# Kernel tuning notes

Hardware: AMD Instinct MI355X
Metric: run time of the kernel (lower is better)

The kernel has to match this reference:

```python
import jax, jax.numpy as jnp
import numpy as np

D_MODEL, FFN, N_EXP = 1024, 4096, 8
BS, L = 4, 2048


def setup_inputs() -> dict:
    key = jax.random.key(0)
    ks = jax.random.split(key, 7)
    s = 0.02
    return {
        "x": jax.random.normal(ks[0], (BS, L, D_MODEL), dtype=jnp.float32),
        "gate_w": s * jax.random.normal(ks[1], (D_MODEL, N_EXP), dtype=jnp.float32),
        "gate_b": jnp.zeros((N_EXP,), dtype=jnp.float32),
        "W1": s * jax.random.normal(ks[2], (N_EXP, D_MODEL, FFN), dtype=jnp.float32),
        "b1": jnp.zeros((N_EXP, FFN), dtype=jnp.float32),
        "W2": s * jax.random.normal(ks[3], (N_EXP, FFN, D_MODEL), dtype=jnp.float32),
        "b2": jnp.zeros((N_EXP, D_MODEL), dtype=jnp.float32),
    }


def reference(x, gate_w, gate_b, W1, b1, W2, b2):
    # gate logits [bs, l, E]; NOTE: original applies Softmax(dim=1) -> over seq dim
    logits = jnp.einsum("bld,de->ble", x, gate_w) + gate_b
    probs = jax.nn.softmax(logits, axis=1)  # faithful to nn.Softmax(dim=1)
    idx = jnp.argmax(probs, axis=-1)  # top-1 expert per token, [bs, l]
    # topk_weights are computed in the original but never applied to output.
    out = jnp.zeros_like(x)
    for e in range(N_EXP):  # fixed small expert loop (structurally distinct weights)
        h = jax.nn.gelu(jnp.einsum("bld,df->blf", x, W1[e]) + b1[e], approximate=False)
        y = jnp.einsum("blf,fd->bld", h, W2[e]) + b2[e]
        out = out + jnp.where((idx == e)[..., None], y, jnp.float32(0.0))
    return out
```

## Files before the change

### kernel.cpp

```cpp
#include <hip/hip_runtime.h>
#include <hip/hip_bf16.h>

typedef unsigned short u16;
typedef unsigned int u32;

using bf16x8 = __attribute__((ext_vector_type(8))) short;
using f32x4  = __attribute__((ext_vector_type(4))) float;

static constexpr int TOK  = 8192;
static constexpr int SEQ  = 2048;
static constexpr int DM   = 1024;
static constexpr int FF   = 4096;
static constexpr int NE   = 8;
static constexpr int MAXT = 72;
static constexpr int NT1  = FF/128;
static constexpr int NT2  = DM/128;

static constexpr size_t O_LOGITS = 0;
static constexpr size_t O_M      = 262144;
static constexpr size_t O_Z      = O_M + 128;
static constexpr size_t O_CNT    = O_Z + 128;
static constexpr size_t O_CUR    = O_CNT + 64;
static constexpr size_t O_OFF    = O_CUR + 64;
static constexpr size_t O_DESC   = 263168;
static constexpr size_t O_PERM   = 266240;
static constexpr size_t O_IDX    = 299008;
static constexpr size_t O_XG     = 524288;
static constexpr size_t O_W1T    = O_XG  + (size_t)TOK*DM*2;
static constexpr size_t O_W2T    = O_W1T + (size_t)NE*DM*FF*2;
static constexpr size_t O_H      = O_W2T + (size_t)NE*DM*FF*2;

__device__ __forceinline__ u16 f2bf(float f){
  __hip_bfloat16 h = __float2bfloat16(f);
  return *reinterpret_cast<u16*>(&h);
}

__device__ __forceinline__ void gld_lds16(const void* g, void* l){
  __builtin_amdgcn_global_load_lds((const __attribute__((address_space(1))) void*)g,
                                   (__attribute__((address_space(3))) void*)l, 16, 0, 0);
}

__device__ __forceinline__ float gelu_f(float v){
  float u = v * fmaf(v*v, 0.044715f, 1.0f) * 0.7978845608f;
  float ex = __builtin_amdgcn_exp2f(u * -2.885390082f);
  return v * __builtin_amdgcn_rcpf(1.0f + ex);
}

__global__ void k_gate(const float* __restrict__ x, const float* __restrict__ gw,
                       const float* __restrict__ gb, float* __restrict__ logits){
  __shared__ float sgw[DM*NE];
  for (int i = threadIdx.x; i < DM*NE; i += 256) sgw[i] = gw[i];
  __syncthreads();
  int wave = threadIdx.x >> 6, lane = threadIdx.x & 63;
  int t = blockIdx.x * 4 + wave;
  const float* xr = x + (size_t)t * DM;
  float acc[NE];
#pragma unroll
  for (int e = 0; e < NE; ++e) acc[e] = 0.f;
#pragma unroll
  for (int k = 0; k < 16; ++k){
    int d = k*64 + lane;
    float xv = xr[d];
    const float* g = &sgw[d*NE];
#pragma unroll
    for (int e = 0; e < NE; ++e) acc[e] = fmaf(xv, g[e], acc[e]);
  }
#pragma unroll
  for (int off = 32; off; off >>= 1)
#pragma unroll
    for (int e = 0; e < NE; ++e) acc[e] += __shfl_xor(acc[e], off);
  if (lane == 0){
#pragma unroll
    for (int e = 0; e < NE; ++e) logits[(size_t)t*NE + e] = acc[e] + gb[e];
  }
}

__global__ void k_lse(const float* __restrict__ logits, float* __restrict__ mOut,
                      float* __restrict__ zOut){
  int be = blockIdx.x;
  int b = be >> 3, e = be & 7;
  const float* base = logits + ((size_t)b*SEQ)*NE + e;
  float m = -INFINITY;
  for (int l = threadIdx.x; l < SEQ; l += 256) m = fmaxf(m, base[(size_t)l*NE]);
  __shared__ float red[8];
#pragma unroll
  for (int off = 32; off; off >>= 1) m = fmaxf(m, __shfl_xor(m, off));
  if ((threadIdx.x & 63) == 0) red[threadIdx.x >> 6] = m;
  __syncthreads();
  m = fmaxf(fmaxf(red[0], red[1]), fmaxf(red[2], red[3]));
  float s = 0.f;
  for (int l = threadIdx.x; l < SEQ; l += 256) s += expf(base[(size_t)l*NE] - m);
#pragma unroll
  for (int off = 32; off; off >>= 1) s += __shfl_xor(s, off);
  if ((threadIdx.x & 63) == 0) red[4 + (threadIdx.x >> 6)] = s;
  __syncthreads();
  if (threadIdx.x == 0){ mOut[be] = m; zOut[be] = red[4]+red[5]+red[6]+red[7]; }
}

__global__ void k_route(const float* __restrict__ logits, const float* __restrict__ m,
                        const float* __restrict__ z, u32* __restrict__ cnt,
                        int* __restrict__ idx){
  int t = blockIdx.x*256 + threadIdx.x;
  int b = t >> 11;
  const float* lr = logits + (size_t)t*NE;
  float best = -INFINITY; int be = 0;
#pragma unroll
  for (int e = 0; e < NE; ++e){
    float p = expf(lr[e] - m[b*NE + e]) / z[b*NE + e];
    if (p > best){ best = p; be = e; }
  }
  idx[t] = be;
  atomicAdd(&cnt[be], 1u);
}

__global__ void k_plan(const u32* __restrict__ cnt, int* __restrict__ off,
                       int4* __restrict__ desc, u32* __restrict__ cur){
  if (threadIdx.x == 0){
    int offs[NE+1]; int o = 0;
    for (int e = 0; e < NE; ++e){ offs[e] = o; o += (int)cnt[e]; }
    offs[NE] = o;
    int nt = 0;
    for (int e = 0; e < NE; ++e){
      int c = (int)cnt[e];
      for (int s = 0; s < c; s += 128)
        desc[nt++] = make_int4(e, offs[e] + s, min(128, c - s), 0);
      off[e] = offs[e]; cur[e] = 0u;
    }
    off[NE] = offs[NE];
    for (int i = nt; i < MAXT; ++i) desc[i] = make_int4(-1, 0, 0, 0);
  }
}

__global__ void k_scatter(const int* __restrict__ idx, const int* __restrict__ off,
                          u32* __restrict__ cur, int* __restrict__ perm){
  int t = blockIdx.x*256 + threadIdx.x;
  int e = idx[t];
  int pos = off[e] + (int)atomicAdd(&cur[e], 1u);
  perm[pos] = t;
}

__global__ void k_gather(const float* __restrict__ x, const int* __restrict__ perm,
                         u16* __restrict__ Xg){
  int p = blockIdx.x;
  int t = perm[p];
  const float4* src = (const float4*)(x + (size_t)t*DM);
  float4 v = src[threadIdx.x];
  uint2 o;
  o.x = (u32)f2bf(v.x) | ((u32)f2bf(v.y) << 16);
  o.y = (u32)f2bf(v.z) | ((u32)f2bf(v.w) << 16);
  *(uint2*)(Xg + (size_t)p*DM + threadIdx.x*4) = o;
}

__global__ void k_trans(const float* __restrict__ in, u16* __restrict__ out,
                        int R, int C){
  __shared__ float tile[64][65];
  int e = blockIdx.z;
  int r0 = blockIdx.x*64, c0 = blockIdx.y*64;
  const float* src = in + ((size_t)e*R + r0)*C + c0;
  int lr = threadIdx.x >> 4, lc = (threadIdx.x & 15) * 4;
#pragma unroll
  for (int i = 0; i < 4; ++i){
    float4 v = *(const float4*)(src + (size_t)(lr + i*16)*C + lc);
    tile[lr + i*16][lc+0] = v.x; tile[lr + i*16][lc+1] = v.y;
    tile[lr + i*16][lc+2] = v.z; tile[lr + i*16][lc+3] = v.w;
  }
  __syncthreads();
  u16* dst = out + ((size_t)e*C + c0)*R + r0;
#pragma unroll
  for (int i = 0; i < 4; ++i){
    int oc = lr + i*16;
    u16 a0 = f2bf(tile[lc+0][oc]);
    u16 a1 = f2bf(tile[lc+1][oc]);
    u16 a2 = f2bf(tile[lc+2][oc]);
    u16 a3 = f2bf(tile[lc+3][oc]);
    uint2 o; o.x = (u32)a0 | ((u32)a1 << 16); o.y = (u32)a2 | ((u32)a3 << 16);
    *(uint2*)(dst + (size_t)oc*R + lc) = o;
  }
}

__global__ __launch_bounds__(256) void k_ffn1(const u16* __restrict__ Xg,
    const u16* __restrict__ W1T, const float* __restrict__ b1,
    u16* __restrict__ H, const int4* __restrict__ desc){
  int pid = blockIdx.x;
  int pid_sw = (pid & 7) * (MAXT*NT1/8) + (pid >> 3);
  int mt = pid_sw % MAXT;
  int n0 = (pid_sw / MAXT) * 128;
  int4 dd = desc[mt];
  int e = dd.x; if (e < 0) return;
  int m0 = dd.y, valid = dd.z;
  __shared__ __align__(16) u16 lA[2][128*32];
  __shared__ __align__(16) u16 lB[2][128*32];
  int tid = threadIdx.x, lane = tid & 63, wave = tid >> 6;
  int wr = wave >> 1, wc = wave & 1;
  const u16* Bsrc = W1T + ((size_t)e*FF + n0)*DM;
  f32x4 acc[4][4] = {};

  auto stage = [&](int buf, int kt){
    int k0 = kt * 32;
#pragma unroll
    for (int i = 0; i < 2; ++i){
      int qbase = wave*512 + i*2048;
      int qe = qbase + lane*8;
      int row = qe >> 5, col = qe & 31;
      int rowg = m0 + row; if (rowg > TOK-1) rowg = TOK-1;
      gld_lds16(Xg + (size_t)rowg*DM + k0 + col, &lA[buf][qbase]);
      gld_lds16(Bsrc + (size_t)row*DM + k0 + col, &lB[buf][qbase]);
    }
  };

  stage(0, 0);
  __syncthreads();
  const int KT = DM / 32;
  for (int kt = 0; kt < KT; ++kt){
    int cur = kt & 1;
    if (kt + 1 < KT) stage(cur ^ 1, kt + 1);
    const u16* pa = &lA[cur][(wr*64 + (lane & 15))*32 + (lane >> 4)*8];
    const u16* pb = &lB[cur][(wc*64 + (lane & 15))*32 + (lane >> 4)*8];
    bf16x8 a[4], b[4];
#pragma unroll
    for (int m = 0; m < 4; ++m) a[m] = *(const bf16x8*)(pa + m*16*32);
#pragma unroll
    for (int n = 0; n < 4; ++n) b[n] = *(const bf16x8*)(pb + n*16*32);
#pragma unroll
    for (int m = 0; m < 4; ++m)
#pragma unroll
      for (int n = 0; n < 4; ++n)
        acc[m][n] = __builtin_amdgcn_mfma_f32_16x16x32_bf16(a[m], b[n], acc[m][n], 0, 0, 0);
    __syncthreads();
  }

#pragma unroll
  for (int n = 0; n < 4; ++n){
    int col = n0 + wc*64 + n*16 + (lane & 15);
    float bias = b1[(size_t)e*FF + col];
#pragma unroll
    for (int m = 0; m < 4; ++m){
      int rbase = wr*64 + m*16 + ((lane >> 4) << 2);
#pragma unroll
      for (int j = 0; j < 4; ++j){
        int rit = rbase + j;
        if (rit < valid){
          float v = acc[m][n][j] + bias;
          H[(size_t)(m0 + rit)*FF + col] = f2bf(gelu_f(v));
        }
      }
    }
  }
}

__global__ __launch_bounds__(256) void k_ffn2(const u16* __restrict__ H,
    const u16* __restrict__ W2T, const float* __restrict__ b2,
    float* __restrict__ out, const int4* __restrict__ desc,
    const int* __restrict__ perm){
  int pid = blockIdx.x;
  int pid_sw = (pid & 7) * (MAXT*NT2/8) + (pid >> 3);
  int mt = pid_sw % MAXT;
  int n0 = (pid_sw / MAXT) * 128;
  int4 dd = desc[mt];
  int e = dd.x; if (e < 0) return;
  int m0 = dd.y, valid = dd.z;
  __shared__ __align__(16) u16 lA[2][128*32];
  __shared__ __align__(16) u16 lB[2][128*32];
  int tid = threadIdx.x, lane = tid & 63, wave = tid >> 6;
  int wr = wave >> 1, wc = wave & 1;
  const u16* Bsrc = W2T + ((size_t)e*DM + n0)*FF;
  f32x4 acc[4][4] = {};

  auto stage = [&](int buf, int kt){
    int k0 = kt * 32;
#pragma unroll
    for (int i = 0; i < 2; ++i){
      int qbase = wave*512 + i*2048;
      int qe = qbase + lane*8;
      int row = qe >> 5, col = qe & 31;
      int rowg = m0 + row; if (rowg > TOK-1) rowg = TOK-1;
      gld_lds16(H + (size_t)rowg*FF + k0 + col, &lA[buf][qbase]);
      gld_lds16(Bsrc + (size_t)row*FF + k0 + col, &lB[buf][qbase]);
    }
  };

  stage(0, 0);
  __syncthreads();
  const int KT = FF / 32;
  for (int kt = 0; kt < KT; ++kt){
    int cur = kt & 1;
    if (kt + 1 < KT) stage(cur ^ 1, kt + 1);
    const u16* pa = &lA[cur][(wr*64 + (lane & 15))*32 + (lane >> 4)*8];
    const u16* pb = &lB[cur][(wc*64 + (lane & 15))*32 + (lane >> 4)*8];
    bf16x8 a[4], b[4];
#pragma unroll
    for (int m = 0; m < 4; ++m) a[m] = *(const bf16x8*)(pa + m*16*32);
#pragma unroll
    for (int n = 0; n < 4; ++n) b[n] = *(const bf16x8*)(pb + n*16*32);
#pragma unroll
    for (int m = 0; m < 4; ++m)
#pragma unroll
      for (int n = 0; n < 4; ++n)
        acc[m][n] = __builtin_amdgcn_mfma_f32_16x16x32_bf16(a[m], b[n], acc[m][n], 0, 0, 0);
    __syncthreads();
  }

#pragma unroll
  for (int m = 0; m < 4; ++m){
#pragma unroll
    for (int j = 0; j < 4; ++j){
      int rit = wr*64 + m*16 + ((lane >> 4) << 2) + j;
      if (rit < valid){
        int tok = perm[m0 + rit];
#pragma unroll
        for (int n = 0; n < 4; ++n){
          int col = n0 + wc*64 + n*16 + (lane & 15);
          out[(size_t)tok*DM + col] = acc[m][n][j] + b2[(size_t)e*DM + col];
        }
      }
    }
  }
}

extern "C" void kernel_launch(void* const* d_in, const int* in_sizes, int n_in,
                              void* d_out, int out_size, void* d_ws, size_t ws_size,
                              hipStream_t stream){
  const float* x   = (const float*)d_in[0];
  const float* gw  = (const float*)d_in[1];
  const float* gb  = (const float*)d_in[2];
  const float* W1  = (const float*)d_in[3];
  const float* b1  = (const float*)d_in[4];
  const float* W2  = (const float*)d_in[5];
  const float* b2  = (const float*)d_in[6];
  float* out = (float*)d_out;
  char* ws = (char*)d_ws;

  float* logits = (float*)(ws + O_LOGITS);
  float* mArr   = (float*)(ws + O_M);
  float* zArr   = (float*)(ws + O_Z);
  u32*   cnt    = (u32*)  (ws + O_CNT);
  u32*   cur    = (u32*)  (ws + O_CUR);
  int*   off    = (int*)  (ws + O_OFF);
  int4*  desc   = (int4*) (ws + O_DESC);
  int*   perm   = (int*)  (ws + O_PERM);
  int*   idx    = (int*)  (ws + O_IDX);
  u16*   Xg     = (u16*)  (ws + O_XG);
  u16*   W1T    = (u16*)  (ws + O_W1T);
  u16*   W2T    = (u16*)  (ws + O_W2T);
  u16*   Hbuf   = (u16*)  (ws + O_H);

  hipMemsetAsync(ws + O_CNT, 0, 128, stream);

  k_gate   <<<TOK/4, 256, 0, stream>>>(x, gw, gb, logits);
  k_lse    <<<32,    256, 0, stream>>>(logits, mArr, zArr);
  k_route  <<<TOK/256, 256, 0, stream>>>(logits, mArr, zArr, cnt, idx);
  k_plan   <<<1,     64,  0, stream>>>(cnt, off, desc, cur);
  k_scatter<<<TOK/256, 256, 0, stream>>>(idx, off, cur, perm);
  k_gather <<<TOK,   256, 0, stream>>>(x, perm, Xg);
  k_trans  <<<dim3(DM/64, FF/64, NE), 256, 0, stream>>>(W1, W1T, DM, FF);
  k_trans  <<<dim3(FF/64, DM/64, NE), 256, 0, stream>>>(W2, W2T, FF, DM);
  k_ffn1   <<<MAXT*NT1, 256, 0, stream>>>(Xg, W1T, b1, Hbuf, desc);
  k_ffn2   <<<MAXT*NT2, 256, 0, stream>>>(Hbuf, W2T, b2, out, desc, perm);
}
```

Baseline: 474.6 us.

## Enlarge FFN1 tiles to 256x256 with swizzled LDS and split-K FFN2

FFN1 moves to 256x256 output tiles with a 64-wide K step and 512 threads. It adds an XOR-swizzled LDS layout, a phased MFMA schedule with raw barriers and setprio, and a second tile descriptor list built from 256-row chunks. FFN2 splits K in two and accumulates into the output with atomic adds, after a new kernel prefills the output with the per-expert bias. The aim is more data reuse per tile in the large GEMM and more workgroups for the small-N second GEMM. The cost is larger LDS use, heavier padding waste on partial 256-row tiles, and atomic traffic on the output.

```diff
diff --git a/kernel.cpp b/kernel.cpp
--- a/kernel.cpp
+++ b/kernel.cpp
@@ -13,8 +13,11 @@
 static constexpr int FF   = 4096;
 static constexpr int NE   = 8;
 static constexpr int MAXT = 72;
-static constexpr int NT1  = FF/128;
+static constexpr int MAXT2= 40;
 static constexpr int NT2  = DM/128;
+static constexpr int KS2  = 2;
+static constexpr int NWG1 = MAXT2 * (FF/256);
+static constexpr int NWG2 = MAXT * NT2 * KS2;
 
 static constexpr size_t O_LOGITS = 0;
 static constexpr size_t O_M      = 262144;
@@ -23,6 +26,7 @@
 static constexpr size_t O_CUR    = O_CNT + 64;
 static constexpr size_t O_OFF    = O_CUR + 64;
 static constexpr size_t O_DESC   = 263168;
+static constexpr size_t O_DESC2  = 264320;
 static constexpr size_t O_PERM   = 266240;
 static constexpr size_t O_IDX    = 299008;
 static constexpr size_t O_XG     = 524288;
@@ -39,6 +43,9 @@
   __builtin_amdgcn_global_load_lds((const __attribute__((address_space(1))) void*)g,
                                    (__attribute__((address_space(3))) void*)l, 16, 0, 0);
 }
+
+#define BAR()    asm volatile("s_barrier" ::: "memory")
+#define WAITV0() asm volatile("s_waitcnt vmcnt(0)" ::: "memory")
 
 __device__ __forceinline__ float gelu_f(float v){
   float u = v * fmaf(v*v, 0.044715f, 1.0f) * 0.7978845608f;
@@ -114,20 +121,24 @@
 }
 
 __global__ void k_plan(const u32* __restrict__ cnt, int* __restrict__ off,
-                       int4* __restrict__ desc, u32* __restrict__ cur){
+                       int4* __restrict__ desc, int4* __restrict__ desc2,
+                       u32* __restrict__ cur){
   if (threadIdx.x == 0){
     int offs[NE+1]; int o = 0;
     for (int e = 0; e < NE; ++e){ offs[e] = o; o += (int)cnt[e]; }
     offs[NE] = o;
-    int nt = 0;
+    int nt = 0, nt2 = 0;
     for (int e = 0; e < NE; ++e){
       int c = (int)cnt[e];
       for (int s = 0; s < c; s += 128)
         desc[nt++] = make_int4(e, offs[e] + s, min(128, c - s), 0);
+      for (int s = 0; s < c; s += 256)
+        desc2[nt2++] = make_int4(e, offs[e] + s, min(256, c - s), 0);
       off[e] = offs[e]; cur[e] = 0u;
     }
     off[NE] = offs[NE];
-    for (int i = nt; i < MAXT; ++i) desc[i] = make_int4(-1, 0, 0, 0);
+    for (int i = nt;  i < MAXT;  ++i) desc[i]  = make_int4(-1, 0, 0, 0);
+    for (int i = nt2; i < MAXT2; ++i) desc2[i] = make_int4(-1, 0, 0, 0);
   }
 }
 
@@ -178,69 +189,105 @@
   }
 }
 
-__global__ __launch_bounds__(256) void k_ffn1(const u16* __restrict__ Xg,
+__global__ __launch_bounds__(512, 2) void k_ffn1(const u16* __restrict__ Xg,
     const u16* __restrict__ W1T, const float* __restrict__ b1,
-    u16* __restrict__ H, const int4* __restrict__ desc){
+    u16* __restrict__ H, const int4* __restrict__ desc2){
   int pid = blockIdx.x;
-  int pid_sw = (pid & 7) * (MAXT*NT1/8) + (pid >> 3);
-  int mt = pid_sw % MAXT;
-  int n0 = (pid_sw / MAXT) * 128;
-  int4 dd = desc[mt];
+  int pid_sw = (pid & 7) * (NWG1/8) + (pid >> 3);
+  int mt = pid_sw % MAXT2;
+  int n0 = (pid_sw / MAXT2) * 256;
+  int4 dd = desc2[mt];
   int e = dd.x; if (e < 0) return;
   int m0 = dd.y, valid = dd.z;
-  __shared__ __align__(16) u16 lA[2][128*32];
-  __shared__ __align__(16) u16 lB[2][128*32];
+
+  __shared__ __align__(16) u16 lA[2][256*64];
+  __shared__ __align__(16) u16 lB[2][256*64];
+
   int tid = threadIdx.x, lane = tid & 63, wave = tid >> 6;
-  int wr = wave >> 1, wc = wave & 1;
+  int wm = wave >> 2, wn = wave & 3;
   const u16* Bsrc = W1T + ((size_t)e*FF + n0)*DM;
-  f32x4 acc[4][4] = {};
-
-  auto stage = [&](int buf, int kt){
-    int k0 = kt * 32;
-#pragma unroll
-    for (int i = 0; i < 2; ++i){
-      int qbase = wave*512 + i*2048;
-      int qe = qbase + lane*8;
-      int row = qe >> 5, col = qe & 31;
-      int rowg = m0 + row; if (rowg > TOK-1) rowg = TOK-1;
-      gld_lds16(Xg + (size_t)rowg*DM + k0 + col, &lA[buf][qbase]);
-      gld_lds16(Bsrc + (size_t)row*DM + k0 + col, &lB[buf][qbase]);
+
+  f32x4 acc[8][4] = {};
+  bf16x8 a[4][2], b0[2][2], b1r[2][2];
+
+  int srow = lane >> 3;
+  int cole = ((lane & 7) ^ srow) << 3;
+
+  auto STAGE = [&](int buf, int kt){
+    int k0 = kt * 64;
+    char* dA = (char*)&lA[buf][0];
+    char* dB = (char*)&lB[buf][0];
+#pragma unroll
+    for (int c = 0; c < 4; ++c){
+      int ci = wave*4 + c;
+      int row = ci*8 + srow;
+      int ra = m0 + row; if (ra > TOK-1) ra = TOK-1;
+      gld_lds16(Xg   + (size_t)ra *DM + k0 + cole, dA + ci*1024);
+      gld_lds16(Bsrc + (size_t)row*DM + k0 + cole, dB + ci*1024);
     }
   };
-
-  stage(0, 0);
-  __syncthreads();
-  const int KT = DM / 32;
+  auto LDA = [&](const u16* tb, int half){
+#pragma unroll
+    for (int f = 0; f < 4; ++f){
+      int R = wm*128 + half*64 + f*16 + (lane & 15);
+      int base = R*128 + (((lane >> 4)*16) ^ ((R & 7) << 4));
+      a[f][0] = *(const bf16x8*)((const char*)tb + base);
+      a[f][1] = *(const bf16x8*)((const char*)tb + (base ^ 64));
+    }
+  };
+  auto LDB = [&](const u16* tb, int half, bf16x8 (&b)[2][2]){
+#pragma unroll
+    for (int f = 0; f < 2; ++f){
+      int R = wn*64 + half*32 + f*16 + (lane & 15);
+      int base = R*128 + (((lane >> 4)*16) ^ ((R & 7) << 4));
+      b[f][0] = *(const bf16x8*)((const char*)tb + base);
+      b[f][1] = *(const bf16x8*)((const char*)tb + (base ^ 64));
+    }
+  };
+  auto MM = [&](int mh, int nh, bf16x8 (&b)[2][2]){
+    __builtin_amdgcn_s_setprio(1);
+#pragma unroll
+    for (int f = 0; f < 4; ++f)
+#pragma unroll
+      for (int g = 0; g < 2; ++g){
+        acc[mh*4+f][nh*2+g] =
+          __builtin_amdgcn_mfma_f32_16x16x32_bf16(a[f][0], b[g][0], acc[mh*4+f][nh*2+g], 0,0,0);
+        acc[mh*4+f][nh*2+g] =
+          __builtin_amdgcn_mfma_f32_16x16x32_bf16(a[f][1], b[g][1], acc[mh*4+f][nh*2+g], 0,0,0);
+      }
+    __builtin_amdgcn_s_setprio(0);
+  };
+
+  STAGE(0, 0);
+  WAITV0(); BAR();
+  const int KT = DM / 64;
   for (int kt = 0; kt < KT; ++kt){
-    int cur = kt & 1;
-    if (kt + 1 < KT) stage(cur ^ 1, kt + 1);
-    const u16* pa = &lA[cur][(wr*64 + (lane & 15))*32 + (lane >> 4)*8];
-    const u16* pb = &lB[cur][(wc*64 + (lane & 15))*32 + (lane >> 4)*8];
-    bf16x8 a[4], b[4];
-#pragma unroll
-    for (int m = 0; m < 4; ++m) a[m] = *(const bf16x8*)(pa + m*16*32);
-#pragma unroll
-    for (int n = 0; n < 4; ++n) b[n] = *(const bf16x8*)(pb + n*16*32);
-#pragma unroll
-    for (int m = 0; m < 4; ++m)
-#pragma unroll
-      for (int n = 0; n < 4; ++n)
-        acc[m][n] = __builtin_amdgcn_mfma_f32_16x16x32_bf16(a[m], b[n], acc[m][n], 0, 0, 0);
-    __syncthreads();
-  }
-
-#pragma unroll
-  for (int n = 0; n < 4; ++n){
-    int col = n0 + wc*64 + n*16 + (lane & 15);
+    const u16* cA = &lA[kt & 1][0];
+    const u16* cB = &lB[kt & 1][0];
+    if (kt + 1 < KT) STAGE((kt & 1) ^ 1, kt + 1);
+    LDA(cA, 0); LDB(cB, 0, b0);
+    BAR(); MM(0, 0, b0);  BAR();
+    LDB(cB, 1, b1r);
+    BAR(); MM(0, 1, b1r); BAR();
+    LDA(cA, 1);
+    BAR(); MM(1, 1, b1r); BAR();
+    MM(1, 0, b0);
+    if (kt + 1 < KT) WAITV0();
+    BAR();
+  }
+
+#pragma unroll
+  for (int fn = 0; fn < 4; ++fn){
+    int col = n0 + wn*64 + fn*16 + (lane & 15);
     float bias = b1[(size_t)e*FF + col];
 #pragma unroll
-    for (int m = 0; m < 4; ++m){
-      int rbase = wr*64 + m*16 + ((lane >> 4) << 2);
+    for (int fm = 0; fm < 8; ++fm){
+      int rbase = wm*128 + fm*16 + ((lane >> 4) << 2);
 #pragma unroll
       for (int j = 0; j < 4; ++j){
         int rit = rbase + j;
         if (rit < valid){
-          float v = acc[m][n][j] + bias;
+          float v = acc[fm][fn][j] + bias;
           H[(size_t)(m0 + rit)*FF + col] = f2bf(gelu_f(v));
         }
       }
@@ -248,14 +295,23 @@
   }
 }
 
+__global__ void k_bias(const int* __restrict__ idx, const float* __restrict__ b2,
+                       float* __restrict__ out){
+  int t = blockIdx.x;
+  int e = idx[t];
+  float4 v = *(const float4*)(b2 + (size_t)e*DM + threadIdx.x*4);
+  *(float4*)(out + (size_t)t*DM + threadIdx.x*4) = v;
+}
+
 __global__ __launch_bounds__(256) void k_ffn2(const u16* __restrict__ H,
-    const u16* __restrict__ W2T, const float* __restrict__ b2,
-    float* __restrict__ out, const int4* __restrict__ desc,
-    const int* __restrict__ perm){
+    const u16* __restrict__ W2T, float* __restrict__ out,
+    const int4* __restrict__ desc, const int* __restrict__ perm){
   int pid = blockIdx.x;
-  int pid_sw = (pid & 7) * (MAXT*NT2/8) + (pid >> 3);
+  int pid_sw = (pid & 7) * (NWG2/8) + (pid >> 3);
   int mt = pid_sw % MAXT;
-  int n0 = (pid_sw / MAXT) * 128;
+  int rest = pid_sw / MAXT;
+  int n0 = (rest & 7) * 128;
+  int ks = rest >> 3;
   int4 dd = desc[mt];
   int e = dd.x; if (e < 0) return;
   int m0 = dd.y, valid = dd.z;
@@ -279,12 +335,12 @@
     }
   };
 
-  stage(0, 0);
+  const int k_beg = ks * 64, k_end = k_beg + 64;
+  stage(0, k_beg);
   __syncthreads();
-  const int KT = FF / 32;
-  for (int kt = 0; kt < KT; ++kt){
+  for (int kt = k_beg; kt < k_end; ++kt){
     int cur = kt & 1;
-    if (kt + 1 < KT) stage(cur ^ 1, kt + 1);
+    if (kt + 1 < k_end) stage(cur ^ 1, kt + 1);
     const u16* pa = &lA[cur][(wr*64 + (lane & 15))*32 + (lane >> 4)*8];
     const u16* pb = &lB[cur][(wc*64 + (lane & 15))*32 + (lane >> 4)*8];
     bf16x8 a[4], b[4];
@@ -310,7 +366,7 @@
 #pragma unroll
         for (int n = 0; n < 4; ++n){
           int col = n0 + wc*64 + n*16 + (lane & 15);
-          out[(size_t)tok*DM + col] = acc[m][n][j] + b2[(size_t)e*DM + col];
+          unsafeAtomicAdd(&out[(size_t)tok*DM + col], acc[m][n][j]);
         }
       }
     }
@@ -337,6 +393,7 @@
   u32*   cur    = (u32*)  (ws + O_CUR);
   int*   off    = (int*)  (ws + O_OFF);
   int4*  desc   = (int4*) (ws + O_DESC);
+  int4*  desc2  = (int4*) (ws + O_DESC2);
   int*   perm   = (int*)  (ws + O_PERM);
   int*   idx    = (int*)  (ws + O_IDX);
   u16*   Xg     = (u16*)  (ws + O_XG);
@@ -349,11 +406,12 @@
   k_gate   <<<TOK/4, 256, 0, stream>>>(x, gw, gb, logits);
   k_lse    <<<32,    256, 0, stream>>>(logits, mArr, zArr);
   k_route  <<<TOK/256, 256, 0, stream>>>(logits, mArr, zArr, cnt, idx);
-  k_plan   <<<1,     64,  0, stream>>>(cnt, off, desc, cur);
+  k_plan   <<<1,     64,  0, stream>>>(cnt, off, desc, desc2, cur);
   k_scatter<<<TOK/256, 256, 0, stream>>>(idx, off, cur, perm);
   k_gather <<<TOK,   256, 0, stream>>>(x, perm, Xg);
   k_trans  <<<dim3(DM/64, FF/64, NE), 256, 0, stream>>>(W1, W1T, DM, FF);
   k_trans  <<<dim3(FF/64, DM/64, NE), 256, 0, stream>>>(W2, W2T, FF, DM);
-  k_ffn1   <<<MAXT*NT1, 256, 0, stream>>>(Xg, W1T, b1, Hbuf, desc);
-  k_ffn2   <<<MAXT*NT2, 256, 0, stream>>>(Hbuf, W2T, b2, out, desc, perm);
-}
+  k_ffn1   <<<NWG1,  512, 0, stream>>>(Xg, W1T, b1, Hbuf, desc2);
+  k_bias   <<<TOK,   256, 0, stream>>>(idx, b2, out);
+  k_ffn2   <<<NWG2,  256, 0, stream>>>(Hbuf, W2T, out, desc, perm);
+}
```

Result: slower. 548.7 us (+15.6%).

## Split-K the second expert GEMM with atomic accumulation and rework block ordering

Applied to the files above, without the earlier changes.

The second FFN GEMM is split four ways along K, so the grid is four times larger and each block runs a quarter of the K loop. Partial sums go to the output with float atomic adds. The output is pre-filled with the b2 bias in the gather kernel. The first GEMM's block-to-tile mapping is changed so groups of 8 N-tiles share an M-tile, which targets L2 reuse, and the gate kernel's weights are laid out transposed to allow float4 loads. The cost is atomic traffic and non-deterministic summation order in the output.

```diff
diff --git a/kernel.cpp b/kernel.cpp
--- a/kernel.cpp
+++ b/kernel.cpp
@@ -13,8 +13,9 @@
 static constexpr int FF   = 4096;
 static constexpr int NE   = 8;
 static constexpr int MAXT = 72;
-static constexpr int NT1  = FF/128;
-static constexpr int NT2  = DM/128;
+static constexpr int KS2  = 4;
+static constexpr int NWG1 = MAXT * (FF/128);
+static constexpr int NWG2 = MAXT * (DM/128) * KS2;
 
 static constexpr size_t O_LOGITS = 0;
 static constexpr size_t O_M      = 262144;
@@ -48,22 +49,27 @@
 
 __global__ void k_gate(const float* __restrict__ x, const float* __restrict__ gw,
                        const float* __restrict__ gb, float* __restrict__ logits){
-  __shared__ float sgw[DM*NE];
-  for (int i = threadIdx.x; i < DM*NE; i += 256) sgw[i] = gw[i];
+  __shared__ float sgw[NE*DM];
+  for (int i = threadIdx.x; i < DM*NE; i += 256){
+    int d = i >> 3, e = i & 7;
+    sgw[e*DM + d] = gw[i];
+  }
   __syncthreads();
   int wave = threadIdx.x >> 6, lane = threadIdx.x & 63;
   int t = blockIdx.x * 4 + wave;
-  const float* xr = x + (size_t)t * DM;
+  const float4* xr = (const float4*)(x + (size_t)t * DM);
   float acc[NE];
 #pragma unroll
   for (int e = 0; e < NE; ++e) acc[e] = 0.f;
 #pragma unroll
-  for (int k = 0; k < 16; ++k){
-    int d = k*64 + lane;
-    float xv = xr[d];
-    const float* g = &sgw[d*NE];
-#pragma unroll
-    for (int e = 0; e < NE; ++e) acc[e] = fmaf(xv, g[e], acc[e]);
+  for (int k = 0; k < 4; ++k){
+    int v4 = k*64 + lane;
+    float4 v = xr[v4];
+#pragma unroll
+    for (int e = 0; e < NE; ++e){
+      const float4 g = *(const float4*)&sgw[e*DM + v4*4];
+      acc[e] = fmaf(v.x, g.x, fmaf(v.y, g.y, fmaf(v.z, g.z, fmaf(v.w, g.w, acc[e]))));
+    }
   }
 #pragma unroll
   for (int off = 32; off; off >>= 1)
@@ -140,15 +146,19 @@
 }
 
 __global__ void k_gather(const float* __restrict__ x, const int* __restrict__ perm,
-                         u16* __restrict__ Xg){
+                         const int* __restrict__ idx, const float* __restrict__ b2,
+                         u16* __restrict__ Xg, float* __restrict__ out){
   int p = blockIdx.x;
   int t = perm[p];
+  int e = idx[t];
   const float4* src = (const float4*)(x + (size_t)t*DM);
   float4 v = src[threadIdx.x];
   uint2 o;
   o.x = (u32)f2bf(v.x) | ((u32)f2bf(v.y) << 16);
   o.y = (u32)f2bf(v.z) | ((u32)f2bf(v.w) << 16);
   *(uint2*)(Xg + (size_t)p*DM + threadIdx.x*4) = o;
+  float4 bv = ((const float4*)(b2 + (size_t)e*DM))[threadIdx.x];
+  ((float4*)(out + (size_t)t*DM))[threadIdx.x] = bv;
 }
 
 __global__ void k_trans(const float* __restrict__ in, u16* __restrict__ out,
@@ -178,13 +188,16 @@
   }
 }
 
+
 __global__ __launch_bounds__(256) void k_ffn1(const u16* __restrict__ Xg,
     const u16* __restrict__ W1T, const float* __restrict__ b1,
     u16* __restrict__ H, const int4* __restrict__ desc){
   int pid = blockIdx.x;
-  int pid_sw = (pid & 7) * (MAXT*NT1/8) + (pid >> 3);
-  int mt = pid_sw % MAXT;
-  int n0 = (pid_sw / MAXT) * 128;
+  int pid_sw = (pid & 7) * (NWG1/8) + (pid >> 3);
+  int ng  = pid_sw / (MAXT*8);
+  int rem = pid_sw - ng*(MAXT*8);
+  int mt  = rem >> 3;
+  int n0  = (ng*8 + (rem & 7)) * 128;
   int4 dd = desc[mt];
   int e = dd.x; if (e < 0) return;
   int m0 = dd.y, valid = dd.z;
@@ -249,13 +262,14 @@
 }
 
 __global__ __launch_bounds__(256) void k_ffn2(const u16* __restrict__ H,
-    const u16* __restrict__ W2T, const float* __restrict__ b2,
-    float* __restrict__ out, const int4* __restrict__ desc,
-    const int* __restrict__ perm){
+    const u16* __restrict__ W2T, float* __restrict__ out,
+    const int4* __restrict__ desc, const int* __restrict__ perm){
   int pid = blockIdx.x;
-  int pid_sw = (pid & 7) * (MAXT*NT2/8) + (pid >> 3);
-  int mt = pid_sw % MAXT;
-  int n0 = (pid_sw / MAXT) * 128;
+  int pid_sw = (pid & 7) * (NWG2/8) + (pid >> 3);
+  int ks  = pid_sw / (MAXT*8);
+  int rem = pid_sw - ks*(MAXT*8);
+  int mt  = rem >> 3;
+  int n0  = (rem & 7) * 128;
   int4 dd = desc[mt];
   int e = dd.x; if (e < 0) return;
   int m0 = dd.y, valid = dd.z;
@@ -264,10 +278,11 @@
   int tid = threadIdx.x, lane = tid & 63, wave = tid >> 6;
   int wr = wave >> 1, wc = wave & 1;
   const u16* Bsrc = W2T + ((size_t)e*DM + n0)*FF;
+  const int kbase = ks * (FF/KS2);
   f32x4 acc[4][4] = {};
 
   auto stage = [&](int buf, int kt){
-    int k0 = kt * 32;
+    int k0 = kbase + kt * 32;
 #pragma unroll
     for (int i = 0; i < 2; ++i){
       int qbase = wave*512 + i*2048;
@@ -281,7 +296,7 @@
 
   stage(0, 0);
   __syncthreads();
-  const int KT = FF / 32;
+  const int KT = (FF/KS2) / 32;
   for (int kt = 0; kt < KT; ++kt){
     int cur = kt & 1;
     if (kt + 1 < KT) stage(cur ^ 1, kt + 1);
@@ -310,7 +325,7 @@
 #pragma unroll
         for (int n = 0; n < 4; ++n){
           int col = n0 + wc*64 + n*16 + (lane & 15);
-          out[(size_t)tok*DM + col] = acc[m][n][j] + b2[(size_t)e*DM + col];
+          unsafeAtomicAdd(&out[(size_t)tok*DM + col], acc[m][n][j]);
         }
       }
     }
@@ -351,9 +366,9 @@
   k_route  <<<TOK/256, 256, 0, stream>>>(logits, mArr, zArr, cnt, idx);
   k_plan   <<<1,     64,  0, stream>>>(cnt, off, desc, cur);
   k_scatter<<<TOK/256, 256, 0, stream>>>(idx, off, cur, perm);
-  k_gather <<<TOK,   256, 0, stream>>>(x, perm, Xg);
+  k_gather <<<TOK,   256, 0, stream>>>(x, perm, idx, b2, Xg, out);
   k_trans  <<<dim3(DM/64, FF/64, NE), 256, 0, stream>>>(W1, W1T, DM, FF);
   k_trans  <<<dim3(FF/64, DM/64, NE), 256, 0, stream>>>(W2, W2T, FF, DM);
-  k_ffn1   <<<MAXT*NT1, 256, 0, stream>>>(Xg, W1T, b1, Hbuf, desc);
-  k_ffn2   <<<MAXT*NT2, 256, 0, stream>>>(Hbuf, W2T, b2, out, desc, perm);
-}
+  k_ffn1   <<<NWG1,  256, 0, stream>>>(Xg, W1T, b1, Hbuf, desc);
+  k_ffn2   <<<NWG2,  256, 0, stream>>>(Hbuf, W2T, out, desc, perm);
+}
```

New measurement: 510.7 us. 1.08x slower.
